# Kernel tuning notes

Measured on AMD Instinct MI355X. Metric: run time of the kernel, lower is better.

The kernel has to match this reference:

```python
import jax, jax.numpy as jnp
import numpy as np

B, S, E, H = 2, 2048, 1024, 16
D = E // H  # head dim = 64


def setup_inputs() -> dict:
    key = jax.random.key(0)
    ks = jax.random.split(key, 8)
    return {
        "query": jax.random.normal(ks[0], (B, S, E), dtype=jnp.float32),
        "key": jax.random.normal(ks[1], (B, S, E), dtype=jnp.float32),
        "value": jax.random.normal(ks[2], (B, S, E), dtype=jnp.float32),
        "qkv_weight": jax.random.normal(ks[3], (3 * E, E), dtype=jnp.float32) * 0.02,
        "qkv_bias": jax.random.normal(ks[4], (3 * E,), dtype=jnp.float32) * 0.02,
        "proj_weight": jax.random.normal(ks[5], (E, E), dtype=jnp.float32) * 0.02,
        "proj_bias": jax.random.normal(ks[6], (E,), dtype=jnp.float32) * 0.02,
        "mask": jax.random.normal(ks[7], (S, S), dtype=jnp.float32),
    }


def reference(query, key, value, qkv_weight, qkv_bias, proj_weight, proj_bias, mask):
    # Split fused QKV weight/bias into per-projection chunks ([E,E] each).
    wq, wk, wv = jnp.split(qkv_weight, 3, axis=0)
    bq, bk, bv = jnp.split(qkv_bias, 3, axis=0)

    def proj_heads(x, w, b):
        # [B,S,E] @ [E,E]^T + [E] -> [B,H,S,D]
        y = jnp.einsum("bse,fe->bsf", x, w) + b
        return y.reshape(B, S, H, D).transpose(0, 2, 1, 3)

    q = proj_heads(query, wq, bq)
    k = proj_heads(key, wk, bk)
    v = proj_heads(value, wv, bv)

    scale = 1.0 / jnp.sqrt(jnp.asarray(D, dtype=q.dtype))
    # scores: [B,H,S,S]; mask_type 0 -> additive [S,S] float mask broadcast over B,H
    scores = jnp.einsum("bhsd,bhtd->bhst", q, k) * scale + mask[None, None, :, :]
    attn = jax.nn.softmax(scores, axis=-1)
    ctx = jnp.einsum("bhst,bhtd->bhsd", attn, v)  # [B,H,S,D]
    ctx = ctx.transpose(0, 2, 1, 3).reshape(B, S, E)
    # output projection
    return jnp.einsum("bse,fe->bsf", ctx, proj_weight) + proj_bias
```

## Files before the change

kernel.cpp:

```cpp
#include <hip/hip_runtime.h>
#include <hip/hip_bf16.h>

typedef unsigned short u16;
typedef __attribute__((ext_vector_type(8))) __bf16 bf16x8;
typedef __attribute__((ext_vector_type(4))) __bf16 bf16x4;
typedef __attribute__((ext_vector_type(4))) float f32x4;

#define LOG2E 1.44269504f

#if __has_builtin(__builtin_amdgcn_exp2f)
#define EXP2F(x) __builtin_amdgcn_exp2f(x)
#else
#define EXP2F(x) __expf((x) * 0.69314718f)
#endif

#define GLL16(gptr, lptr) \
  __builtin_amdgcn_global_load_lds((__attribute__((address_space(1))) void*)(gptr), \
                                   (__attribute__((address_space(3))) void*)(lptr), 16, 0, 0)

static __device__ __forceinline__ u16 f2bf(float f) {
  union { float f; unsigned u; } v; v.f = f;
  unsigned r = (v.u + 0x7FFFu + ((v.u >> 16) & 1u)) >> 16;
  return (u16)r;
}

__global__ __launch_bounds__(256) void cvt_all(
    const float* __restrict__ q, const float* __restrict__ k, const float* __restrict__ v,
    const float* __restrict__ w1, const float* __restrict__ w2,
    u16* __restrict__ xq, u16* __restrict__ xk, u16* __restrict__ xv,
    u16* __restrict__ wq, u16* __restrict__ wp) {
  const int b = blockIdx.x;
  const float* src; u16* dst; int off;
  if (b < 4096)       { src = q;  dst = xq; off = b; }
  else if (b < 8192)  { src = k;  dst = xk; off = b - 4096; }
  else if (b < 12288) { src = v;  dst = xv; off = b - 8192; }
  else if (b < 15360) { src = w1; dst = wq; off = b - 12288; }
  else                { src = w2; dst = wp; off = b - 15360; }
  const int i = off * 256 + threadIdx.x;
  float4 vv = ((const float4*)src)[i];
  ushort4 o;
  o.x = f2bf(vv.x); o.y = f2bf(vv.y); o.z = f2bf(vv.z); o.w = f2bf(vv.w);
  ((ushort4*)dst)[i] = o;
}

__global__ __launch_bounds__(256, 2) void qkv_gemm(
    const u16* __restrict__ xq, const u16* __restrict__ xk, const u16* __restrict__ xv,
    const u16* __restrict__ wbf, const float* __restrict__ bias,
    u16* __restrict__ qout, u16* __restrict__ kout, u16* __restrict__ vtout) {
  __shared__ u16 Al[128 * 32];
  __shared__ u16 Bl[128 * 32];
  const int tid = threadIdx.x;
  const int lane = tid & 63;
  const int w = tid >> 6;
  const int wr = w >> 1, wc = w & 1;
  const int nb = blockIdx.x, mb = blockIdx.y;
  const int row0 = mb * 128;
  const int ncol0 = nb * 128;
  const int which = nb >> 3;
  const u16* A = (which == 0) ? xq : (which == 1) ? xk : xv;
  const u16* Bw = wbf + (size_t)ncol0 * 1024;

  f32x4 acc[4][4];
  f32x4 zero = {0.f, 0.f, 0.f, 0.f};
#pragma unroll
  for (int i = 0; i < 4; i++)
#pragma unroll
    for (int j = 0; j < 4; j++) acc[i][j] = zero;

  const int srow = w * 16 + (lane >> 2);
  const int scol = (lane & 3) * 8;

  for (int k0 = 0; k0 < 1024; k0 += 32) {
#pragma unroll
    for (int p = 0; p < 2; p++) {
      const u16* ga = A + (size_t)(row0 + p * 64 + srow) * 1024 + k0 + scol;
      GLL16(ga, &Al[(p * 64 + w * 16) * 32]);
      const u16* gb = Bw + (size_t)(p * 64 + srow) * 1024 + k0 + scol;
      GLL16(gb, &Bl[(p * 64 + w * 16) * 32]);
    }
    __syncthreads();
    bf16x8 af[4], bfr[4];
#pragma unroll
    for (int mi = 0; mi < 4; mi++)
      af[mi] = *(const bf16x8*)&Al[(wr * 64 + mi * 16 + (lane & 15)) * 32 + (lane >> 4) * 8];
#pragma unroll
    for (int ni = 0; ni < 4; ni++)
      bfr[ni] = *(const bf16x8*)&Bl[(wc * 64 + ni * 16 + (lane & 15)) * 32 + (lane >> 4) * 8];
#pragma unroll
    for (int mi = 0; mi < 4; mi++)
#pragma unroll
      for (int ni = 0; ni < 4; ni++)
        acc[mi][ni] = __builtin_amdgcn_mfma_f32_16x16x32_bf16(af[mi], bfr[ni], acc[mi][ni], 0, 0, 0);
    __syncthreads();
  }

#pragma unroll
  for (int mi = 0; mi < 4; mi++) {
    const int rb = row0 + wr * 64 + mi * 16 + (lane >> 4) * 4;
#pragma unroll
    for (int ni = 0; ni < 4; ni++) {
      const int c = ncol0 + wc * 64 + ni * 16 + (lane & 15);
      const float bs = bias[c];
      const float sc = (which == 0) ? (0.125f * LOG2E) : 1.0f;
      const int fm = c & 1023;
      const int h = fm >> 6, d = fm & 63;
#pragma unroll
      for (int r = 0; r < 4; r++) {
        const int rr = rb + r;
        const int b = rr >> 11, s = rr & 2047;
        const u16 val = f2bf((acc[mi][ni][r] + bs) * sc);
        if (which == 0)
          qout[(((size_t)(b * 16 + h)) * 2048 + s) * 64 + d] = val;
        else if (which == 1)
          kout[(((size_t)(b * 16 + h)) * 2048 + s) * 64 + d] = val;
        else
          vtout[(((size_t)(b * 16 + h)) * 64 + d) * 2048 + s] = val;
      }
    }
  }
}


#define STAGE_KV(KOFF, VOFF)                                        \
  *(float4*)(ldsb + (KOFF) + S0) = kr0;                             \
  *(float4*)(ldsb + (KOFF) + 4096 + S0) = kr1;                      \
  *(float2*)(ldsb + (VOFF) + VS0a) = make_float2(vr0.x, vr0.y);     \
  *(float2*)(ldsb + (VOFF) + VS0b) = make_float2(vr0.z, vr0.w);     \
  *(float2*)(ldsb + (VOFF) + VS1a) = make_float2(vr1.x, vr1.y);     \
  *(float2*)(ldsb + (VOFF) + VS1b) = make_float2(vr1.z, vr1.w);

#define ATTN_TILE(PAR, MC)                                                         \
  {                                                                                \
    f32x4 s0_, s1_, s2_, s3_;                                                      \
    __builtin_amdgcn_s_setprio(1);                                                 \
    {                                                                              \
      bf16x8 a_, b_;                                                               \
      a_ = *(const bf16x8*)(ldsb + Kr0 + 0 + (PAR));                               \
      b_ = *(const bf16x8*)(ldsb + Kr1 + 0 + (PAR));                               \
      s0_ = __builtin_amdgcn_mfma_f32_16x16x32_bf16(a_, q0, MC[0], 0, 0, 0);       \
      s0_ = __builtin_amdgcn_mfma_f32_16x16x32_bf16(b_, q1, s0_, 0, 0, 0);         \
      a_ = *(const bf16x8*)(ldsb + Kr0 + 2048 + (PAR));                            \
      b_ = *(const bf16x8*)(ldsb + Kr1 + 2048 + (PAR));                            \
      s1_ = __builtin_amdgcn_mfma_f32_16x16x32_bf16(a_, q0, MC[1], 0, 0, 0);       \
      s1_ = __builtin_amdgcn_mfma_f32_16x16x32_bf16(b_, q1, s1_, 0, 0, 0);         \
      a_ = *(const bf16x8*)(ldsb + Kr0 + 4096 + (PAR));                            \
      b_ = *(const bf16x8*)(ldsb + Kr1 + 4096 + (PAR));                            \
      s2_ = __builtin_amdgcn_mfma_f32_16x16x32_bf16(a_, q0, MC[2], 0, 0, 0);       \
      s2_ = __builtin_amdgcn_mfma_f32_16x16x32_bf16(b_, q1, s2_, 0, 0, 0);         \
      a_ = *(const bf16x8*)(ldsb + Kr0 + 6144 + (PAR));                            \
      b_ = *(const bf16x8*)(ldsb + Kr1 + 6144 + (PAR));                            \
      s3_ = __builtin_amdgcn_mfma_f32_16x16x32_bf16(a_, q0, MC[3], 0, 0, 0);       \
      s3_ = __builtin_amdgcn_mfma_f32_16x16x32_bf16(b_, q1, s3_, 0, 0, 0);         \
    }                                                                              \
    __builtin_amdgcn_s_setprio(0);                                                 \
    float pm = fmaxf(fmaxf(fmaxf(fmaxf(s0_[0], s0_[1]), fmaxf(s0_[2], s0_[3])),    \
                           fmaxf(fmaxf(s1_[0], s1_[1]), fmaxf(s1_[2], s1_[3]))),   \
                     fmaxf(fmaxf(fmaxf(s2_[0], s2_[1]), fmaxf(s2_[2], s2_[3])),    \
                           fmaxf(fmaxf(s3_[0], s3_[1]), fmaxf(s3_[2], s3_[3]))));  \
                     \
    s0_[0] = EXP2F(s0_[0] - m); s0_[1] = EXP2F(s0_[1] - m);                        \
    s0_[2] = EXP2F(s0_[2] - m); s0_[3] = EXP2F(s0_[3] - m);                        \
    s1_[0] = EXP2F(s1_[0] - m); s1_[1] = EXP2F(s1_[1] - m);                        \
    s1_[2] = EXP2F(s1_[2] - m); s1_[3] = EXP2F(s1_[3] - m);                        \
    s2_[0] = EXP2F(s2_[0] - m); s2_[1] = EXP2F(s2_[1] - m);                        \
    s2_[2] = EXP2F(s2_[2] - m); s2_[3] = EXP2F(s2_[3] - m);                        \
    s3_[0] = EXP2F(s3_[0] - m); s3_[1] = EXP2F(s3_[1] - m);                        \
    s3_[2] = EXP2F(s3_[2] - m); s3_[3] = EXP2F(s3_[3] - m);                        \
    float ps = ((s0_[0] + s0_[1]) + (s0_[2] + s0_[3])) +                           \
               ((s1_[0] + s1_[1]) + (s1_[2] + s1_[3])) +                           \
               ((s2_[0] + s2_[1]) + (s2_[2] + s2_[3])) +                           \
               ((s3_[0] + s3_[1]) + (s3_[2] + s3_[3]));                            \
    pm = fmaxf(pm, __shfl_xor(pm, 16));                                            \
    pm = fmaxf(pm, __shfl_xor(pm, 32));                                            \
    if (__any(pm > m + 8.0f)) {                 \
      const float mn = fmaxf(m, pm);                                               \
      const float al = EXP2F(m - mn);                                              \
      m = mn; lsum *= al; ps *= al;                                                \
      s0_ *= al; s1_ *= al; s2_ *= al; s3_ *= al;                                  \
      ctx[0] *= al; ctx[1] *= al; ctx[2] *= al; ctx[3] *= al;                      \
    }                                                                              \
    lsum += ps;                                                                    \
           \
    bf16x8 pa0, pa1;                                                               \
    pa0[0] = (__bf16)s0_[0]; pa0[1] = (__bf16)s0_[1];                              \
    pa0[2] = (__bf16)s0_[2]; pa0[3] = (__bf16)s0_[3];                              \
    pa0[4] = (__bf16)s1_[0]; pa0[5] = (__bf16)s1_[1];                              \
    pa0[6] = (__bf16)s1_[2]; pa0[7] = (__bf16)s1_[3];                              \
    pa1[0] = (__bf16)s2_[0]; pa1[1] = (__bf16)s2_[1];                              \
    pa1[2] = (__bf16)s2_[2]; pa1[3] = (__bf16)s2_[3];                              \
    pa1[4] = (__bf16)s3_[0]; pa1[5] = (__bf16)s3_[1];                              \
    pa1[6] = (__bf16)s3_[2]; pa1[7] = (__bf16)s3_[3];                              \
    {                                                                              \
      bf16x8 v00 = *(const bf16x8*)(ldsb + Kr0 + 16384 + (PAR));                   \
      bf16x8 v01 = *(const bf16x8*)(ldsb + Kr1 + 16384 + (PAR));                   \
      bf16x8 v10 = *(const bf16x8*)(ldsb + Kr0 + 18432 + (PAR));                   \
      bf16x8 v11 = *(const bf16x8*)(ldsb + Kr1 + 18432 + (PAR));                   \
      bf16x8 v20 = *(const bf16x8*)(ldsb + Kr0 + 20480 + (PAR));                   \
      bf16x8 v21 = *(const bf16x8*)(ldsb + Kr1 + 20480 + (PAR));                   \
      bf16x8 v30 = *(const bf16x8*)(ldsb + Kr0 + 22528 + (PAR));                   \
      bf16x8 v31 = *(const bf16x8*)(ldsb + Kr1 + 22528 + (PAR));                   \
      __builtin_amdgcn_s_setprio(1);                                               \
      ctx[0] = __builtin_amdgcn_mfma_f32_16x16x32_bf16(v00, pa0, ctx[0], 0, 0, 0); \
      ctx[0] = __builtin_amdgcn_mfma_f32_16x16x32_bf16(v01, pa1, ctx[0], 0, 0, 0); \
      ctx[1] = __builtin_amdgcn_mfma_f32_16x16x32_bf16(v10, pa0, ctx[1], 0, 0, 0); \
      ctx[1] = __builtin_amdgcn_mfma_f32_16x16x32_bf16(v11, pa1, ctx[1], 0, 0, 0); \
      ctx[2] = __builtin_amdgcn_mfma_f32_16x16x32_bf16(v20, pa0, ctx[2], 0, 0, 0); \
      ctx[2] = __builtin_amdgcn_mfma_f32_16x16x32_bf16(v21, pa1, ctx[2], 0, 0, 0); \
      ctx[3] = __builtin_amdgcn_mfma_f32_16x16x32_bf16(v30, pa0, ctx[3], 0, 0, 0); \
      ctx[3] = __builtin_amdgcn_mfma_f32_16x16x32_bf16(v31, pa1, ctx[3], 0, 0, 0); \
      __builtin_amdgcn_s_setprio(0);                                               \
    }                                                                              \
  }

__global__ __launch_bounds__(256, 4) void attn_fwd(
    const u16* __restrict__ qbf, const u16* __restrict__ kbf, const u16* __restrict__ vtbf,
    const float* __restrict__ mask, u16* __restrict__ ctxout) {
  __shared__ u16 lds[16384];
  char* ldsb = (char*)lds;
  const int tid = threadIdx.x, lane = tid & 63, w = tid >> 6;
  const int qL = lane & 15, g = lane >> 4;
  const int x = (qL & 7) << 4;
  const int bh = blockIdx.x, qt = blockIdx.y;
  const int qbase = qt * 64;
  const size_t hbase = (size_t)bh * 2048 * 64;
  const int qrow = qbase + w * 16 + qL;

  const int Kr0 = qL * 128 + ((g * 16) ^ x);
  const int Kr1 = qL * 128 + ((g * 16 + 64) ^ x);
  const int srow = tid >> 3;
  const int scol = (tid & 7) * 8;
  const int S0 = srow * 128 + (((tid & 7) * 16) ^ ((srow & 7) << 4));
  const int a_ = tid & 7;
  const int vW1 = ((a_ >> 2) << 6) + (((2 * a_) & 3) << 4) + (((a_ >> 1) & 1) << 3);
  const int vW2 = ((a_ >> 2) << 6) + (((2 * a_ + 1) & 3) << 4) + (((a_ >> 1) & 1) << 3);
  const int sxr = (srow & 7) << 4;
  const int VS0a = srow * 128 + (vW1 ^ sxr);
  const int VS0b = srow * 128 + (vW2 ^ sxr);
  const int VS1a = (32 + srow) * 128 + (vW1 ^ sxr);
  const int VS1b = (32 + srow) * 128 + (vW2 ^ sxr);

  bf16x8 q0 = *(const bf16x8*)&qbf[hbase + (size_t)qrow * 64 + g * 8];
  bf16x8 q1 = *(const bf16x8*)&qbf[hbase + (size_t)qrow * 64 + 32 + g * 8];

  float4 kr0, kr1, vr0, vr1;
  kr0 = *(const float4*)&kbf[hbase + (size_t)srow * 64 + scol];
  kr1 = *(const float4*)&kbf[hbase + (size_t)(32 + srow) * 64 + scol];
  vr0 = *(const float4*)&vtbf[hbase + (size_t)srow * 2048 + scol];
  vr1 = *(const float4*)&vtbf[hbase + (size_t)(32 + srow) * 2048 + scol];
  STAGE_KV(0, 16384)
  kr0 = *(const float4*)&kbf[hbase + (size_t)(64 + srow) * 64 + scol];
  kr1 = *(const float4*)&kbf[hbase + (size_t)(96 + srow) * 64 + scol];
  vr0 = *(const float4*)&vtbf[hbase + (size_t)srow * 2048 + 64 + scol];
  vr1 = *(const float4*)&vtbf[hbase + (size_t)(32 + srow) * 2048 + 64 + scol];

  const u16* kpA = kbf + hbase + (size_t)(128 + srow) * 64 + scol;
  const u16* kpB = kbf + hbase + (size_t)(160 + srow) * 64 + scol;
  const u16* vpA = vtbf + hbase + (size_t)srow * 2048 + 128 + scol;
  const u16* vpB = vtbf + hbase + (size_t)(32 + srow) * 2048 + 128 + scol;
  const float* mp = mask + (size_t)qrow * 2048 + g * 4;

  f32x4 mA[4], mB[4];
#pragma unroll
  for (int tb = 0; tb < 4; tb++)
    mA[tb] = (*(const f32x4*)(mp + tb * 16)) * LOG2E;

  float m = 0.f, lsum = 0.f;
  f32x4 ctx[4];
  f32x4 zero = {0.f, 0.f, 0.f, 0.f};
#pragma unroll
  for (int db = 0; db < 4; db++) ctx[db] = zero;

  __syncthreads();

  for (int i = 0; i < 16; ++i) {
    STAGE_KV(8192, 24576)
    if (i < 15) {
      kr0 = *(const float4*)kpA;
      kr1 = *(const float4*)kpB;
      vr0 = *(const float4*)vpA;
      vr1 = *(const float4*)vpB;
      kpA += 4096; kpB += 4096; vpA += 64; vpB += 64;
    }
#pragma unroll
    for (int tb = 0; tb < 4; tb++)
      mB[tb] = (*(const f32x4*)(mp + 64 + tb * 16)) * LOG2E;
    ATTN_TILE(0, mA)
    __syncthreads();

    if (i < 15) {
      STAGE_KV(0, 16384)
      kr0 = *(const float4*)kpA;
      kr1 = *(const float4*)kpB;
      vr0 = *(const float4*)vpA;
      vr1 = *(const float4*)vpB;
      kpA += 4096; kpB += 4096; vpA += 64; vpB += 64;
#pragma unroll
      for (int tb = 0; tb < 4; tb++)
        mA[tb] = (*(const f32x4*)(mp + 128 + tb * 16)) * LOG2E;
    }
    ATTN_TILE(8192, mB)
    mp += 128;
    __syncthreads();
  }

  lsum += __shfl_xor(lsum, 16);
  lsum += __shfl_xor(lsum, 32);
  const float inv = 1.0f / lsum;
  const int b = bh >> 4, h = bh & 15;
  u16* orow = ctxout + (size_t)(b * 2048 + qrow) * 1024 + h * 64;
#pragma unroll
  for (int db = 0; db < 4; db++) {
    bf16x4 o;
    o[0] = (__bf16)(ctx[db][0] * inv);
    o[1] = (__bf16)(ctx[db][1] * inv);
    o[2] = (__bf16)(ctx[db][2] * inv);
    o[3] = (__bf16)(ctx[db][3] * inv);
    *(bf16x4*)&orow[db * 16 + g * 4] = o;
  }
}

__global__ __launch_bounds__(256, 2) void proj_gemm(
    const u16* __restrict__ ctx, const u16* __restrict__ wbf,
    const float* __restrict__ bias, float* __restrict__ out) {
  __shared__ u16 Al[128 * 32];
  __shared__ u16 Bl[128 * 32];
  const int tid = threadIdx.x;
  const int lane = tid & 63;
  const int w = tid >> 6;
  const int wr = w >> 1, wc = w & 1;
  const int nb = blockIdx.x, mb = blockIdx.y;
  const int row0 = mb * 128;
  const int ncol0 = nb * 128;
  const u16* Bw = wbf + (size_t)ncol0 * 1024;

  f32x4 acc[4][4];
  f32x4 zero = {0.f, 0.f, 0.f, 0.f};
#pragma unroll
  for (int i = 0; i < 4; i++)
#pragma unroll
    for (int j = 0; j < 4; j++) acc[i][j] = zero;

  const int srow = w * 16 + (lane >> 2);
  const int scol = (lane & 3) * 8;

  for (int k0 = 0; k0 < 1024; k0 += 32) {
#pragma unroll
    for (int p = 0; p < 2; p++) {
      const u16* ga = ctx + (size_t)(row0 + p * 64 + srow) * 1024 + k0 + scol;
      GLL16(ga, &Al[(p * 64 + w * 16) * 32]);
      const u16* gb = Bw + (size_t)(p * 64 + srow) * 1024 + k0 + scol;
      GLL16(gb, &Bl[(p * 64 + w * 16) * 32]);
    }
    __syncthreads();
    bf16x8 af[4], bfr[4];
#pragma unroll
    for (int mi = 0; mi < 4; mi++)
      af[mi] = *(const bf16x8*)&Al[(wr * 64 + mi * 16 + (lane & 15)) * 32 + (lane >> 4) * 8];
#pragma unroll
    for (int ni = 0; ni < 4; ni++)
      bfr[ni] = *(const bf16x8*)&Bl[(wc * 64 + ni * 16 + (lane & 15)) * 32 + (lane >> 4) * 8];
#pragma unroll
    for (int mi = 0; mi < 4; mi++)
#pragma unroll
      for (int ni = 0; ni < 4; ni++)
        acc[mi][ni] = __builtin_amdgcn_mfma_f32_16x16x32_bf16(af[mi], bfr[ni], acc[mi][ni], 0, 0, 0);
    __syncthreads();
  }

#pragma unroll
  for (int mi = 0; mi < 4; mi++) {
    const int rb = row0 + wr * 64 + mi * 16 + (lane >> 4) * 4;
#pragma unroll
    for (int ni = 0; ni < 4; ni++) {
      const int c = ncol0 + wc * 64 + ni * 16 + (lane & 15);
      const float bs = bias[c];
#pragma unroll
      for (int r = 0; r < 4; r++)
        out[(size_t)(rb + r) * 1024 + c] = acc[mi][ni][r] + bs;
    }
  }
}

extern "C" void kernel_launch(void* const* d_in, const int* in_sizes, int n_in,
                              void* d_out, int out_size, void* d_ws, size_t ws_size,
                              hipStream_t stream) {
  const float* query = (const float*)d_in[0];
  const float* key   = (const float*)d_in[1];
  const float* value = (const float*)d_in[2];
  const float* qkvw  = (const float*)d_in[3];
  const float* qkvb  = (const float*)d_in[4];
  const float* projw = (const float*)d_in[5];
  const float* projb = (const float*)d_in[6];
  const float* mask  = (const float*)d_in[7];

  char* ws = (char*)d_ws;
  u16* xq    = (u16*)(ws + 0);
  u16* xk    = (u16*)(ws + 8388608);
  u16* xv    = (u16*)(ws + 16777216);
  u16* wqkv  = (u16*)(ws + 25165824);
  u16* wproj = (u16*)(ws + 31457280);
  u16* qb    = (u16*)(ws + 33554432);
  u16* kb    = (u16*)(ws + 41943040);
  u16* vt    = (u16*)(ws + 50331648);
  u16* cx    = xq;

  cvt_all<<<16384, 256, 0, stream>>>(query, key, value, qkvw, projw, xq, xk, xv, wqkv, wproj);
  qkv_gemm<<<dim3(24, 32), 256, 0, stream>>>(xq, xk, xv, wqkv, qkvb, qb, kb, vt);
  attn_fwd<<<dim3(32, 32), 256, 0, stream>>>(qb, kb, vt, mask, cx);
  proj_gemm<<<dim3(8, 32), 256, 0, stream>>>(cx, wproj, projb, (float*)d_out);
}
```

Measured before the change: 193.5 us.

## Double attention query tile to 128 rows with 512-thread blocks sharing K/V staging

The attention kernel now runs 8 waves per block over 128 query rows instead of 4 waves over 64. Each thread stages half as much K/V data per tile, and the shared K/V tile is reused across twice as many query rows. This halves global K/V traffic per query and the number of blocks. In exchange, the larger blocks and heavier barrier synchronisation may reduce occupancy and scheduling flexibility.

```diff
diff --git a/kernel.cpp b/kernel.cpp
--- a/kernel.cpp
+++ b/kernel.cpp
@@ -123,11 +123,8 @@
 
 #define STAGE_KV(KOFF, VOFF)                                        \
   *(float4*)(ldsb + (KOFF) + S0) = kr0;                             \
-  *(float4*)(ldsb + (KOFF) + 4096 + S0) = kr1;                      \
   *(float2*)(ldsb + (VOFF) + VS0a) = make_float2(vr0.x, vr0.y);     \
-  *(float2*)(ldsb + (VOFF) + VS0b) = make_float2(vr0.z, vr0.w);     \
-  *(float2*)(ldsb + (VOFF) + VS1a) = make_float2(vr1.x, vr1.y);     \
-  *(float2*)(ldsb + (VOFF) + VS1b) = make_float2(vr1.z, vr1.w);
+  *(float2*)(ldsb + (VOFF) + VS0b) = make_float2(vr0.z, vr0.w);
 
 #define ATTN_TILE(PAR, MC)                                                         \
   {                                                                                \
@@ -212,7 +209,7 @@
     }                                                                              \
   }
 
-__global__ __launch_bounds__(256, 4) void attn_fwd(
+__global__ __launch_bounds__(512, 4) void attn_fwd(
     const u16* __restrict__ qbf, const u16* __restrict__ kbf, const u16* __restrict__ vtbf,
     const float* __restrict__ mask, u16* __restrict__ ctxout) {
   __shared__ u16 lds[16384];
@@ -221,7 +218,7 @@
   const int qL = lane & 15, g = lane >> 4;
   const int x = (qL & 7) << 4;
   const int bh = blockIdx.x, qt = blockIdx.y;
-  const int qbase = qt * 64;
+  const int qbase = qt * 128;
   const size_t hbase = (size_t)bh * 2048 * 64;
   const int qrow = qbase + w * 16 + qL;
 
@@ -236,27 +233,19 @@
   const int sxr = (srow & 7) << 4;
   const int VS0a = srow * 128 + (vW1 ^ sxr);
   const int VS0b = srow * 128 + (vW2 ^ sxr);
-  const int VS1a = (32 + srow) * 128 + (vW1 ^ sxr);
-  const int VS1b = (32 + srow) * 128 + (vW2 ^ sxr);
 
   bf16x8 q0 = *(const bf16x8*)&qbf[hbase + (size_t)qrow * 64 + g * 8];
   bf16x8 q1 = *(const bf16x8*)&qbf[hbase + (size_t)qrow * 64 + 32 + g * 8];
 
-  float4 kr0, kr1, vr0, vr1;
+  float4 kr0, vr0;
   kr0 = *(const float4*)&kbf[hbase + (size_t)srow * 64 + scol];
-  kr1 = *(const float4*)&kbf[hbase + (size_t)(32 + srow) * 64 + scol];
   vr0 = *(const float4*)&vtbf[hbase + (size_t)srow * 2048 + scol];
-  vr1 = *(const float4*)&vtbf[hbase + (size_t)(32 + srow) * 2048 + scol];
   STAGE_KV(0, 16384)
   kr0 = *(const float4*)&kbf[hbase + (size_t)(64 + srow) * 64 + scol];
-  kr1 = *(const float4*)&kbf[hbase + (size_t)(96 + srow) * 64 + scol];
   vr0 = *(const float4*)&vtbf[hbase + (size_t)srow * 2048 + 64 + scol];
-  vr1 = *(const float4*)&vtbf[hbase + (size_t)(32 + srow) * 2048 + 64 + scol];
-
-  const u16* kpA = kbf + hbase + (size_t)(128 + srow) * 64 + scol;
-  const u16* kpB = kbf + hbase + (size_t)(160 + srow) * 64 + scol;
-  const u16* vpA = vtbf + hbase + (size_t)srow * 2048 + 128 + scol;
-  const u16* vpB = vtbf + hbase + (size_t)(32 + srow) * 2048 + 128 + scol;
+
+  const u16* kp = kbf + hbase + (size_t)(128 + srow) * 64 + scol;
+  const u16* vp = vtbf + hbase + (size_t)srow * 2048 + 128 + scol;
   const float* mp = mask + (size_t)qrow * 2048 + g * 4;
 
   f32x4 mA[4], mB[4];
@@ -275,11 +264,9 @@
   for (int i = 0; i < 16; ++i) {
     STAGE_KV(8192, 24576)
     if (i < 15) {
-      kr0 = *(const float4*)kpA;
-      kr1 = *(const float4*)kpB;
-      vr0 = *(const float4*)vpA;
-      vr1 = *(const float4*)vpB;
-      kpA += 4096; kpB += 4096; vpA += 64; vpB += 64;
+      kr0 = *(const float4*)kp;
+      vr0 = *(const float4*)vp;
+      kp += 4096; vp += 64;
     }
 #pragma unroll
     for (int tb = 0; tb < 4; tb++)
@@ -289,11 +276,9 @@
 
     if (i < 15) {
       STAGE_KV(0, 16384)
-      kr0 = *(const float4*)kpA;
-      kr1 = *(const float4*)kpB;
-      vr0 = *(const float4*)vpA;
-      vr1 = *(const float4*)vpB;
-      kpA += 4096; kpB += 4096; vpA += 64; vpB += 64;
+      kr0 = *(const float4*)kp;
+      vr0 = *(const float4*)vp;
+      kp += 4096; vp += 64;
 #pragma unroll
       for (int tb = 0; tb < 4; tb++)
         mA[tb] = (*(const f32x4*)(mp + 128 + tb * 16)) * LOG2E;
@@ -406,6 +391,6 @@
 
   cvt_all<<<16384, 256, 0, stream>>>(query, key, value, qkvw, projw, xq, xk, xv, wqkv, wproj);
   qkv_gemm<<<dim3(24, 32), 256, 0, stream>>>(xq, xk, xv, wqkv, qkvb, qb, kb, vt);
-  attn_fwd<<<dim3(32, 32), 256, 0, stream>>>(qb, kb, vt, mask, cx);
+  attn_fwd<<<dim3(32, 16), 512, 0, stream>>>(qb, kb, vt, mask, cx);
   proj_gemm<<<dim3(8, 32), 256, 0, stream>>>(cx, wproj, projb, (float*)d_out);
 }
```

Result: faster. 160.9 us (-16.8%).
